# Optimization experiments

Hardware: AMD Instinct MI355X
Metric: run time of the kernel (lower is better)

The kernel has to match this reference:

```python
import jax, jax.numpy as jnp
import numpy as np

N = 10000      # nodes
E = 320000     # edges
H = 128        # hidden_features
GF = 12        # graph-level features
L = 6          # gnn layers
EPS = 1e-5


def _glorot(key, shape):
    fan_in = shape[0]
    return (jax.random.normal(key, shape, jnp.float32) / np.sqrt(fan_in)).astype(jnp.float32)


def periodic_difference(x_i, x_j, domain):
    diff = x_i - x_j
    # (1 - 2*(x_i < x_j)) * domain  ==  +domain if x_i >= x_j else -domain
    shift = jnp.where(x_i < x_j, -domain, domain)
    diff_shifted = diff - shift
    return jnp.where(jnp.abs(diff) < jnp.abs(diff_shifted), diff, diff_shifted)


def _mlp2_relu(x, W1, b1, W2, b2):
    # Linear -> ReLU -> Linear -> ReLU
    return jax.nn.relu(jax.nn.relu(x @ W1 + b1) @ W2 + b2)


def setup_inputs() -> dict:
    key = jax.random.key(0)
    ks = jax.random.split(key, 32)
    inp = {
        "v": jax.random.normal(ks[0], (N, 6), jnp.float32),
        "pos": jax.random.uniform(ks[1], (N, 3), jnp.float32),
        "r": jax.random.uniform(ks[2], (N, 1), jnp.float32),
        "domain": jnp.ones((3,), jnp.float32),
        "t": jax.random.uniform(ks[3], (1,), jnp.float32),
        "x_global": jax.random.normal(ks[4], (4,), jnp.float32),
        "domain_next": jnp.ones((3,), jnp.float32),
        "t_next": jax.random.uniform(ks[5], (1,), jnp.float32),
        "edge_index": jax.random.randint(ks[6], (2, E), 0, N, jnp.int32),
        "batch": jnp.zeros((N,), jnp.int32),
    }
    # embedding MLP: 19 -> H -> H
    inp["emb_W1"] = _glorot(ks[7], (19, H)); inp["emb_b1"] = jnp.zeros((H,), jnp.float32)
    inp["emb_W2"] = _glorot(ks[8], (H, H)); inp["emb_b2"] = jnp.zeros((H,), jnp.float32)
    # per-layer message net: 157 -> H -> H ; update net: 268 -> H -> H
    msg_in = H + GF + 3 + 2 * (6 + 1)   # 157
    upd_in = H + H + GF                 # 268
    inp["msg_W1"] = jnp.stack([_glorot(jax.random.fold_in(ks[9], i), (msg_in, H)) for i in range(L)])
    inp["msg_b1"] = jnp.zeros((L, H), jnp.float32)
    inp["msg_W2"] = jnp.stack([_glorot(jax.random.fold_in(ks[10], i), (H, H)) for i in range(L)])
    inp["msg_b2"] = jnp.zeros((L, H), jnp.float32)
    inp["upd_W1"] = jnp.stack([_glorot(jax.random.fold_in(ks[11], i), (upd_in, H)) for i in range(L)])
    inp["upd_b1"] = jnp.zeros((L, H), jnp.float32)
    inp["upd_W2"] = jnp.stack([_glorot(jax.random.fold_in(ks[12], i), (H, H)) for i in range(L)])
    inp["upd_b2"] = jnp.zeros((L, H), jnp.float32)
    # output MLP: H -> H -> 9 ; macro MLP: H -> H -> 3
    inp["out_W1"] = _glorot(ks[13], (H, H)); inp["out_b1"] = jnp.zeros((H,), jnp.float32)
    inp["out_W2"] = _glorot(ks[14], (H, 9)); inp["out_b2"] = jnp.zeros((9,), jnp.float32)
    inp["mac_W1"] = _glorot(ks[15], (H, H)); inp["mac_b1"] = jnp.zeros((H,), jnp.float32)
    inp["mac_W2"] = _glorot(ks[16], (H, 3)); inp["mac_b2"] = jnp.zeros((3,), jnp.float32)
    return inp


def reference(v, pos, r, domain, t, x_global, domain_next, t_next, edge_index, batch,
              emb_W1, emb_b1, emb_W2, emb_b2,
              msg_W1, msg_b1, msg_W2, msg_b2,
              upd_W1, upd_b1, upd_W2, upd_b2,
              out_W1, out_b1, out_W2, out_b2,
              mac_W1, mac_b1, mac_W2, mac_b2):
    n = v.shape[0]
    gf = jnp.concatenate([domain, t, x_global, domain_next, t_next])          # [12]
    gf_n = jnp.broadcast_to(gf, (n, GF))
    node_features = jnp.concatenate([pos, v], axis=1)                         # [N, 9]

    # embedding (positions excluded)
    h = _mlp2_relu(jnp.concatenate([r, v, gf_n], axis=1), emb_W1, emb_b1, emb_W2, emb_b2)

    src, dst = edge_index[0], edge_index[1]   # j = source, i = target (PyG default)
    gf_e = jnp.broadcast_to(gf, (src.shape[0], GF))
    counts = jax.ops.segment_sum(jnp.ones(src.shape, h.dtype), dst, num_segments=N)
    inv_counts = (1.0 / jnp.maximum(counts, 1.0))[:, None]

    pos_diff = periodic_difference(pos[dst], pos[src], domain)                # [E, 3]
    v_i, v_j, r_i, r_j = v[dst], v[src], r[dst], r[src]

    for l in range(L):
        h_i, h_j = h[dst], h[src]
        msg_in = jnp.concatenate([h_i - h_j, v_i, v_j, r_i, r_j, pos_diff, gf_e], axis=1)
        m = _mlp2_relu(msg_in, msg_W1[l], msg_b1[l], msg_W2[l], msg_b2[l])    # [E, H]
        agg = jax.ops.segment_sum(m, dst, num_segments=N) * inv_counts        # scatter-mean
        upd_in = jnp.concatenate([h, agg, gf_n], axis=1)
        u = _mlp2_relu(upd_in, upd_W1[l], upd_b1[l], upd_W2[l], upd_b2[l])
        h = u + h                                                              # residual (in==out)
        # InstanceNorm over each graph (single graph here), biased variance
        mu = h.mean(axis=0, keepdims=True)
        var = h.var(axis=0, keepdims=True)
        h = (h - mu) / jnp.sqrt(var + EPS)

    prediction = jax.nn.relu(h @ out_W1 + out_b1) @ out_W2 + out_b2 + node_features
    pred_x = jnp.remainder(prediction[:, :3], domain_next)
    pred_v = prediction[:, 3:]
    h_mean = h.mean(axis=0)                                                    # global mean pool, 1 graph
    pred_macro = jax.nn.relu(h_mean @ mac_W1 + mac_b1) @ mac_W2 + mac_b2
    return pred_x, pred_v, pred_macro
```

## Files before the change

kernel.cpp:

```cpp
#include <hip/hip_runtime.h>
#include <hip/hip_bf16.h>

#define NN 10000
#define NE 320000
#define HD 128
#define NL 6
#define EPSV 1e-5f

typedef _Float16 half8  __attribute__((ext_vector_type(8)));
typedef _Float16 half4v __attribute__((ext_vector_type(4)));
typedef float    f32x4  __attribute__((ext_vector_type(4)));

__device__ __forceinline__ float relu_(float x){ return fmaxf(x, 0.0f); }


__global__ void k_degree(const int* __restrict__ dst, int* __restrict__ counts){
  int e = blockIdx.x*256 + threadIdx.x;
  if (e < NE) atomicAdd(&counts[dst[e]], 1);
}

__global__ void k_scan(const int* __restrict__ counts, int* __restrict__ offs, float* __restrict__ invc){
  __shared__ int lds[1024];
  __shared__ int base_s;
  int tid = threadIdx.x;
  if (tid==0) base_s = 0;
  __syncthreads();
  for (int start=0; start<NN; start+=1024){
    int i = start+tid;
    int vv = (i<NN)? counts[i] : 0;
    lds[tid]=vv; __syncthreads();
    for (int off=1; off<1024; off<<=1){
      int t = (tid>=off)? lds[tid-off] : 0;
      __syncthreads();
      lds[tid] += t;
      __syncthreads();
    }
    int incl = lds[tid];
    if (i<NN){
      offs[i] = base_s + incl - vv;
      invc[i] = 1.0f / fmaxf((float)vv, 1.0f);
    }
    __syncthreads();
    if (tid==1023) base_s += lds[1023];
    __syncthreads();
  }
  if (tid==0) offs[NN] = base_s;
}

__global__ void k_place(const int* __restrict__ src, const int* __restrict__ dst,
                        const int* __restrict__ offs, int* __restrict__ cursor, int* __restrict__ csr){
  int e = blockIdx.x*256 + threadIdx.x;
  if (e < NE){
    int d = dst[e];
    int p = atomicAdd(&cursor[d], 1);
    csr[offs[d]+p] = src[e];
  }
}


__global__ void k_biasfold(const float* __restrict__ dom, const float* __restrict__ tt,
                           const float* __restrict__ xg, const float* __restrict__ domn,
                           const float* __restrict__ tn,
                           const float* __restrict__ embW1, const float* __restrict__ embB1,
                           const float* __restrict__ msgW1, const float* __restrict__ msgB1,
                           const float* __restrict__ updW1, const float* __restrict__ updB1,
                           float* __restrict__ b1eff, float* __restrict__ mu, float* __restrict__ rstd){
  float gf[12];
  gf[0]=dom[0]; gf[1]=dom[1]; gf[2]=dom[2]; gf[3]=tt[0];
  gf[4]=xg[0]; gf[5]=xg[1]; gf[6]=xg[2]; gf[7]=xg[3];
  gf[8]=domn[0]; gf[9]=domn[1]; gf[10]=domn[2]; gf[11]=tn[0];
  int b = blockIdx.x, t = threadIdx.x;
  if (b==0){
    float s = embB1[t];
    #pragma unroll
    for (int k=0;k<12;++k) s += gf[k]*embW1[(7+k)*HD + t];
    b1eff[t] = s;
  } else if (b<=6){
    int l=b-1;
    float s = msgB1[l*HD+t];
    #pragma unroll
    for (int k=0;k<12;++k) s += gf[k]*msgW1[((size_t)l*157 + 145+k)*HD + t];
    b1eff[(1+l)*HD + t] = s;
  } else if (b<=12){
    int l=b-7;
    float s = updB1[l*HD+t];
    #pragma unroll
    for (int k=0;k<12;++k) s += gf[k]*updW1[((size_t)l*268 + 256+k)*HD + t];
    b1eff[(7+l)*HD + t] = s;
  } else {
    mu[t] = 0.f;
    rstd[t] = 1.f;
  }
}


__global__ void k_embed(const float* __restrict__ r, const float* __restrict__ v,
                        const float* __restrict__ W1, const float* __restrict__ b1e,
                        const float* __restrict__ W2, const float* __restrict__ b2,
                        float* __restrict__ hb){
  __shared__ alignas(16) float a1s[4][HD];
  int tid=threadIdx.x, wid=tid>>6, lane=tid&63;
  int gw = blockIdx.x*4 + wid;
  int f0=lane, f1=lane+64;
  float* a1 = a1s[wid];
  float b1f0=b1e[f0], b1f1=b1e[f1], b2f0=b2[f0], b2f1=b2[f1];
  for (int n=gw*4; n<gw*4+4; ++n){
    float in7[7];
    in7[0]=r[n];
    #pragma unroll
    for (int k=0;k<6;++k) in7[1+k]=v[n*6+k];
    float z0=b1f0, z1=b1f1;
    #pragma unroll
    for (int k=0;k<7;++k){ z0 += in7[k]*W1[k*HD+f0]; z1 += in7[k]*W1[k*HD+f1]; }
    a1[f0]=relu_(z0); a1[f1]=relu_(z1);
    float h0=b2f0, h1=b2f1;
    for (int k=0;k<HD;++k){ float a=a1[k]; h0+=a*W2[k*HD+f0]; h1+=a*W2[k*HD+f1]; }
    hb[n*HD+f0]=relu_(h0); hb[n*HD+f1]=relu_(h1);
  }
}


__global__ void k_hW(const float* __restrict__ hb, const float* __restrict__ mu, const float* __restrict__ rstd,
                     const float* __restrict__ v, const float* __restrict__ r,
                     const float* __restrict__ W, const float* __restrict__ b1e,
                     float* __restrict__ P, float* __restrict__ Q){
  __shared__ alignas(16) float hs[4][HD*4];
  int tid=threadIdx.x, wid=tid>>6, lane=tid&63;
  int gw=blockIdx.x*4+wid;
  int f0=lane, f1=lane+64;
  float* h4 = hs[wid];
  int n0 = gw*4;
  float mu0=mu[f0], mu1=mu[f1], rs0=rstd[f0], rs1=rstd[f1];
  float4 hv0, hv1;
  hv0.x=(hb[(n0+0)*HD+f0]-mu0)*rs0; hv0.y=(hb[(n0+1)*HD+f0]-mu0)*rs0;
  hv0.z=(hb[(n0+2)*HD+f0]-mu0)*rs0; hv0.w=(hb[(n0+3)*HD+f0]-mu0)*rs0;
  hv1.x=(hb[(n0+0)*HD+f1]-mu1)*rs1; hv1.y=(hb[(n0+1)*HD+f1]-mu1)*rs1;
  hv1.z=(hb[(n0+2)*HD+f1]-mu1)*rs1; hv1.w=(hb[(n0+3)*HD+f1]-mu1)*rs1;
  *(float4*)&h4[f0*4]=hv0; *(float4*)&h4[f1*4]=hv1;
  float m0[4]={0,0,0,0}, m1[4]={0,0,0,0};
  for (int k=0;k<HD;++k){
    float4 a = *(const float4*)&h4[k*4];
    float w0=W[k*HD+f0], w1=W[k*HD+f1];
    m0[0]+=a.x*w0; m1[0]+=a.x*w1;
    m0[1]+=a.y*w0; m1[1]+=a.y*w1;
    m0[2]+=a.z*w0; m1[2]+=a.z*w1;
    m0[3]+=a.w*w0; m1[3]+=a.w*w1;
  }
  float wvi0[6], wvi1[6], wvj0[6], wvj1[6];
  #pragma unroll
  for (int x=0;x<6;++x){
    wvi0[x]=W[(128+x)*HD+f0]; wvi1[x]=W[(128+x)*HD+f1];
    wvj0[x]=W[(134+x)*HD+f0]; wvj1[x]=W[(134+x)*HD+f1];
  }
  float wri0=W[140*HD+f0], wri1=W[140*HD+f1];
  float wrj0=W[141*HD+f0], wrj1=W[141*HD+f1];
  float b10=b1e[f0], b11=b1e[f1];
  #pragma unroll
  for (int e=0;e<4;++e){
    int n = n0+e;
    float p0 = m0[e] + b10, p1 = m1[e] + b11;
    float q0 = -m0[e],      q1 = -m1[e];
    #pragma unroll
    for (int x=0;x<6;++x){
      float vx = v[n*6+x];
      p0 += vx*wvi0[x]; p1 += vx*wvi1[x];
      q0 += vx*wvj0[x]; q1 += vx*wvj1[x];
    }
    float rn = r[n];
    p0 += rn*wri0; p1 += rn*wri1;
    q0 += rn*wrj0; q1 += rn*wrj1;
    P[n*HD+f0]=p0; P[n*HD+f1]=p1;
    Q[n*HD+f0]=q0; Q[n*HD+f1]=q1;
  }
}


__global__ __launch_bounds__(256,2) void k_edge(
    const float* __restrict__ P, const float* __restrict__ Q,
    const float* __restrict__ pos, const float* __restrict__ dom,
    const int* __restrict__ offs, const int* __restrict__ csr,
    const float* __restrict__ Wpd, const float* __restrict__ W2, const float* __restrict__ b2,
    const float* __restrict__ invc, float* __restrict__ agg,
    float* __restrict__ zsum, float* __restrict__ zsumsq){
  __shared__ alignas(16) _Float16 w1pd[128*32];
  __shared__ alignas(16) _Float16 a1hi[16*136];
  __shared__ alignas(16) _Float16 a1lo[16*136];
  int tid = threadIdx.x;
  if (blockIdx.x==0 && tid<HD){ zsum[tid]=0.f; zsumsq[tid]=0.f; }
  if (tid < 128){
    int f = tid;
    #pragma unroll
    for (int k=0;k<32;++k) w1pd[f*32+k] = (_Float16)0.f;
    #pragma unroll
    for (int x=0;x<3;++x){
      float w = Wpd[x*HD + f];
      _Float16 h = (_Float16)w;
      w1pd[f*32 + x]     = h;
      w1pd[f*32 + 3 + x] = h;
      w1pd[f*32 + 6 + x] = (_Float16)(w - (float)h);
    }
  }
  int wid = tid>>6, lane = tid&63, g = lane>>4, c = lane&15;
  int t0 = 2*wid, t1 = 2*wid+1;
  half8 w2h[4][2], w2l[4][2];
  #pragma unroll
  for (int ks=0; ks<4; ++ks){
    #pragma unroll
    for (int tt=0; tt<2; ++tt){
      int col = 16*(2*wid+tt) + c;
      half8 fh, fl;
      #pragma unroll
      for (int j=0;j<8;++j){
        float w = W2[(ks*32 + g*8 + j)*HD + col];
        _Float16 h = (_Float16)w;
        fh[j] = h;
        fl[j] = (_Float16)(w - (float)h);
      }
      w2h[ks][tt] = fh;
      w2l[ks][tt] = fl;
    }
  }
  float b2v0 = b2[16*t0 + c], b2v1 = b2[16*t1 + c];
  float dm0=dom[0], dm1=dom[1], dm2=dom[2];
  f32x4 zero4 = {0.f,0.f,0.f,0.f};
  __syncthreads();
  int n0 = blockIdx.x*4;
  for (int n = n0; n < n0+4; ++n){
    f32x4 pv0 = *(const f32x4*)(P + (size_t)n*HD + 16*t0 + 4*g);
    f32x4 pv1 = *(const f32x4*)(P + (size_t)n*HD + 16*t1 + 4*g);
    float pn0=pos[n*3+0], pn1=pos[n*3+1], pn2=pos[n*3+2];
    float acc0=0.f, acc1=0.f;
    int ib=offs[n], ie=offs[n+1];
    for (int base=ib; base<ie; base+=16){
      int nb = ie - base; if (nb>16) nb = 16;
      int sA = csr[base + ((c<nb)? c : nb-1)];
      float q0=pos[sA*3+0], q1=pos[sA*3+1], q2=pos[sA*3+2];
      float pd0,pd1,pd2;
      { float diff,sh,ds;
        diff=pn0-q0; sh=(pn0<q0)?-dm0:dm0; ds=diff-sh; pd0=(fabsf(diff)<fabsf(ds))?diff:ds;
        diff=pn1-q1; sh=(pn1<q1)?-dm1:dm1; ds=diff-sh; pd1=(fabsf(diff)<fabsf(ds))?diff:ds;
        diff=pn2-q2; sh=(pn2<q2)?-dm2:dm2; ds=diff-sh; pd2=(fabsf(diff)<fabsf(ds))?diff:ds;
      }
      _Float16 p0h = (_Float16)pd0, p1h = (_Float16)pd1, p2h = (_Float16)pd2;
      _Float16 p0l = (_Float16)(pd0 - (float)p0h);
      _Float16 p1l = (_Float16)(pd1 - (float)p1h);
      _Float16 p2l = (_Float16)(pd2 - (float)p2h);
      half8 pdf;
      #pragma unroll
      for (int j=0;j<8;++j) pdf[j]=(_Float16)0.f;
      if (g==0){ pdf[0]=p0h; pdf[1]=p1h; pdf[2]=p2h; pdf[3]=p0l; pdf[4]=p1l; pdf[5]=p2l; pdf[6]=p0h; pdf[7]=p1h; }
      else if (g==1){ pdf[0]=p2h; }
      half8 w1f0 = *(const half8*)&w1pd[(16*t0 + c)*32 + g*8];
      half8 w1f1 = *(const half8*)&w1pd[(16*t1 + c)*32 + g*8];
      f32x4 d0 = __builtin_amdgcn_mfma_f32_16x16x32_f16(w1f0, pdf, zero4, 0,0,0);
      f32x4 d1 = __builtin_amdgcn_mfma_f32_16x16x32_f16(w1f1, pdf, zero4, 0,0,0);
      const float* Qs = Q + (size_t)sA*HD;
      f32x4 qv0 = *(const f32x4*)(Qs + 16*t0 + 4*g);
      f32x4 qv1 = *(const f32x4*)(Qs + 16*t1 + 4*g);
      half4v h0, l0, h1, l1;
      #pragma unroll
      for (int j=0;j<4;++j){
        float a = fmaxf(d0[j] + pv0[j] + qv0[j], 0.f);
        _Float16 hh = (_Float16)a;
        h0[j] = hh; l0[j] = (_Float16)(a - (float)hh);
        float b = fmaxf(d1[j] + pv1[j] + qv1[j], 0.f);
        _Float16 hb2 = (_Float16)b;
        h1[j] = hb2; l1[j] = (_Float16)(b - (float)hb2);
      }
      *(half4v*)&a1hi[c*136 + 16*t0 + 4*g] = h0;
      *(half4v*)&a1lo[c*136 + 16*t0 + 4*g] = l0;
      *(half4v*)&a1hi[c*136 + 16*t1 + 4*g] = h1;
      *(half4v*)&a1lo[c*136 + 16*t1 + 4*g] = l1;
      __syncthreads();
      f32x4 m0 = zero4, m1 = zero4;
      #pragma unroll
      for (int ks=0; ks<4; ++ks){
        half8 ah = *(const half8*)&a1hi[c*136 + ks*32 + g*8];
        half8 al = *(const half8*)&a1lo[c*136 + ks*32 + g*8];
        m0 = __builtin_amdgcn_mfma_f32_16x16x32_f16(ah, w2h[ks][0], m0, 0,0,0);
        m0 = __builtin_amdgcn_mfma_f32_16x16x32_f16(al, w2h[ks][0], m0, 0,0,0);
        m0 = __builtin_amdgcn_mfma_f32_16x16x32_f16(ah, w2l[ks][0], m0, 0,0,0);
        m1 = __builtin_amdgcn_mfma_f32_16x16x32_f16(ah, w2h[ks][1], m1, 0,0,0);
        m1 = __builtin_amdgcn_mfma_f32_16x16x32_f16(al, w2h[ks][1], m1, 0,0,0);
        m1 = __builtin_amdgcn_mfma_f32_16x16x32_f16(ah, w2l[ks][1], m1, 0,0,0);
      }
      if (nb == 16){
        acc0 += fmaxf(m0[0]+b2v0,0.f)+fmaxf(m0[1]+b2v0,0.f)+fmaxf(m0[2]+b2v0,0.f)+fmaxf(m0[3]+b2v0,0.f);
        acc1 += fmaxf(m1[0]+b2v1,0.f)+fmaxf(m1[1]+b2v1,0.f)+fmaxf(m1[2]+b2v1,0.f)+fmaxf(m1[3]+b2v1,0.f);
      } else {
        #pragma unroll
        for (int j=0;j<4;++j){
          if (4*g+j < nb){
            acc0 += fmaxf(m0[j]+b2v0, 0.f);
            acc1 += fmaxf(m1[j]+b2v1, 0.f);
          }
        }
      }
      __syncthreads();
    }
    acc0 += __shfl_xor(acc0, 16); acc0 += __shfl_xor(acc0, 32);
    acc1 += __shfl_xor(acc1, 16); acc1 += __shfl_xor(acc1, 32);
    if (g==0){
      float ic = invc[n];
      agg[n*HD + 16*t0 + c] = acc0*ic;
      agg[n*HD + 16*t1 + c] = acc1*ic;
    }
  }
}


__global__ __launch_bounds__(512,1) void k_upd(
    float* __restrict__ hb, const float* __restrict__ mu, const float* __restrict__ rstd,
    const float* __restrict__ agg,
    const float* __restrict__ U1, const float* __restrict__ b1e,
    const float* __restrict__ U2, const float* __restrict__ bs2,
    float* __restrict__ sum, float* __restrict__ sumsq){
  __shared__ alignas(16) _Float16 Xhi[16*264];
  __shared__ alignas(16) _Float16 Xlo[16*264];
  __shared__ alignas(16) _Float16 Ahi[16*136];
  __shared__ alignas(16) _Float16 Alo[16*136];
  int tid = threadIdx.x;
  int n0 = blockIdx.x*16;
  {
    int node = tid>>5, chunk = tid&31;
    int n = n0 + node;
    int f = chunk*8;
    half8 xh, xl;
    if (f < 128){
      #pragma unroll
      for (int j=0;j<8;++j){
        float x = (hb[(size_t)n*HD + f+j] - mu[f+j]) * rstd[f+j];
        _Float16 h = (_Float16)x;
        xh[j] = h; xl[j] = (_Float16)(x - (float)h);
      }
    } else {
      #pragma unroll
      for (int j=0;j<8;++j){
        float x = agg[(size_t)n*HD + (f-128)+j];
        _Float16 h = (_Float16)x;
        xh[j] = h; xl[j] = (_Float16)(x - (float)h);
      }
    }
    *(half8*)&Xhi[node*264 + f] = xh;
    *(half8*)&Xlo[node*264 + f] = xl;
  }
  int wid = tid>>6, lane = tid&63, g = lane>>4, c = lane&15;
  int col = 16*wid + c;
  half8 b1h[8], b1l[8], b2h[4], b2l[4];
  #pragma unroll
  for (int ks=0; ks<8; ++ks){
    half8 fh, fl;
    #pragma unroll
    for (int j=0;j<8;++j){
      float w = U1[(size_t)(ks*32 + g*8 + j)*HD + col];
      _Float16 h = (_Float16)w;
      fh[j]=h; fl[j]=(_Float16)(w - (float)h);
    }
    b1h[ks]=fh; b1l[ks]=fl;
  }
  #pragma unroll
  for (int ks=0; ks<4; ++ks){
    half8 fh, fl;
    #pragma unroll
    for (int j=0;j<8;++j){
      float w = U2[(size_t)(ks*32 + g*8 + j)*HD + col];
      _Float16 h = (_Float16)w;
      fh[j]=h; fl[j]=(_Float16)(w - (float)h);
    }
    b2h[ks]=fh; b2l[ks]=fl;
  }
  f32x4 zero4 = {0.f,0.f,0.f,0.f};
  __syncthreads();
  f32x4 d = zero4;
  #pragma unroll
  for (int ks=0; ks<8; ++ks){
    half8 ah = *(const half8*)&Xhi[c*264 + ks*32 + g*8];
    half8 al = *(const half8*)&Xlo[c*264 + ks*32 + g*8];
    d = __builtin_amdgcn_mfma_f32_16x16x32_f16(ah, b1h[ks], d, 0,0,0);
    d = __builtin_amdgcn_mfma_f32_16x16x32_f16(al, b1h[ks], d, 0,0,0);
    d = __builtin_amdgcn_mfma_f32_16x16x32_f16(ah, b1l[ks], d, 0,0,0);
  }
  {
    float bb = b1e[col];
    #pragma unroll
    for (int jj=0;jj<4;++jj){
      float a = fmaxf(d[jj] + bb, 0.f);
      _Float16 h = (_Float16)a;
      Ahi[(g*4+jj)*136 + col] = h;
      Alo[(g*4+jj)*136 + col] = (_Float16)(a - (float)h);
    }
  }
  __syncthreads();
  f32x4 u = zero4;
  #pragma unroll
  for (int ks=0; ks<4; ++ks){
    half8 ah = *(const half8*)&Ahi[c*136 + ks*32 + g*8];
    half8 al = *(const half8*)&Alo[c*136 + ks*32 + g*8];
    u = __builtin_amdgcn_mfma_f32_16x16x32_f16(ah, b2h[ks], u, 0,0,0);
    u = __builtin_amdgcn_mfma_f32_16x16x32_f16(al, b2h[ks], u, 0,0,0);
    u = __builtin_amdgcn_mfma_f32_16x16x32_f16(ah, b2l[ks], u, 0,0,0);
  }
  float bc = bs2[col];
  float mc = mu[col], rc = rstd[col];
  float s=0.f, q=0.f;
  #pragma unroll
  for (int jj=0;jj<4;++jj){
    int n = n0 + g*4 + jj;
    float hn = (hb[(size_t)n*HD + col] - mc)*rc;
    float b0 = hn + fmaxf(u[jj] + bc, 0.f);
    hb[(size_t)n*HD + col] = b0;
    s += b0; q += b0*b0;
  }
  s += __shfl_xor(s,16); s += __shfl_xor(s,32);
  q += __shfl_xor(q,16); q += __shfl_xor(q,32);
  if (g==0){
    atomicAdd(&sum[col], s);
    atomicAdd(&sumsq[col], q);
  }
}

__global__ void k_normfin(const float* __restrict__ sum, const float* __restrict__ sumsq,
                          float* __restrict__ mu, float* __restrict__ rstd){
  int t=threadIdx.x;
  float m = sum[t]*(1.0f/NN);
  float var = sumsq[t]*(1.0f/NN) - m*m;
  mu[t]=m;
  rstd[t]=rsqrtf(fmaxf(var,0.0f)+EPSV);
}


__global__ void k_out(const float* __restrict__ hb, const float* __restrict__ mu, const float* __restrict__ rstd,
                      const float* __restrict__ pos, const float* __restrict__ v,
                      const float* __restrict__ W1, const float* __restrict__ b1,
                      const float* __restrict__ W2, const float* __restrict__ b2,
                      const float* __restrict__ domn, float* __restrict__ out){
  __shared__ alignas(16) float hs[4][HD*4];
  __shared__ alignas(16) float a1s[4][HD*4];
  int tid=threadIdx.x, wid=tid>>6, lane=tid&63;
  int gw=blockIdx.x*4+wid;
  int f0=lane, f1=lane+64;
  float* h4=hs[wid];
  float* a1p=a1s[wid];
  int n0=gw*4;
  float mu0=mu[f0], mu1=mu[f1], rs0=rstd[f0], rs1=rstd[f1];
  float4 hv0,hv1;
  hv0.x=(hb[(n0+0)*HD+f0]-mu0)*rs0; hv0.y=(hb[(n0+1)*HD+f0]-mu0)*rs0;
  hv0.z=(hb[(n0+2)*HD+f0]-mu0)*rs0; hv0.w=(hb[(n0+3)*HD+f0]-mu0)*rs0;
  hv1.x=(hb[(n0+0)*HD+f1]-mu1)*rs1; hv1.y=(hb[(n0+1)*HD+f1]-mu1)*rs1;
  hv1.z=(hb[(n0+2)*HD+f1]-mu1)*rs1; hv1.w=(hb[(n0+3)*HD+f1]-mu1)*rs1;
  *(float4*)&h4[f0*4]=hv0; *(float4*)&h4[f1*4]=hv1;
  float b1f0=b1[f0], b1f1=b1[f1];
  float zf0[4]={b1f0,b1f0,b1f0,b1f0}, zf1[4]={b1f1,b1f1,b1f1,b1f1};
  for (int k=0;k<HD;++k){
    float4 a = *(const float4*)&h4[k*4];
    float w0=W1[k*HD+f0], w1=W1[k*HD+f1];
    zf0[0]+=a.x*w0; zf1[0]+=a.x*w1;
    zf0[1]+=a.y*w0; zf1[1]+=a.y*w1;
    zf0[2]+=a.z*w0; zf1[2]+=a.z*w1;
    zf0[3]+=a.w*w0; zf1[3]+=a.w*w1;
  }
  *(float4*)&a1p[f0*4] = make_float4(relu_(zf0[0]),relu_(zf0[1]),relu_(zf0[2]),relu_(zf0[3]));
  *(float4*)&a1p[f1*4] = make_float4(relu_(zf1[0]),relu_(zf1[1]),relu_(zf1[2]),relu_(zf1[3]));
  if (lane < 36){
    int e = lane/9, j = lane - e*9;
    int n = n0+e;
    float p = b2[j];
    for (int k=0;k<HD;++k) p += a1p[k*4+e]*W2[k*9+j];
    if (j<3){
      p += pos[n*3+j];
      float d = domn[j];
      p = p - floorf(p/d)*d;
      out[n*3+j] = p;
    } else {
      p += v[n*6 + (j-3)];
      out[3*NN + n*6 + (j-3)] = p;
    }
  }
}

__global__ void k_macro(const float* __restrict__ sum, const float* __restrict__ mu, const float* __restrict__ rstd,
                        const float* __restrict__ W1, const float* __restrict__ b1,
                        const float* __restrict__ W2, const float* __restrict__ b2,
                        float* __restrict__ out){
  __shared__ float hm[HD];
  __shared__ float as[HD];
  int t=threadIdx.x;
  hm[t] = (sum[t]*(1.0f/NN) - mu[t])*rstd[t];
  __syncthreads();
  float z=b1[t];
  for (int k=0;k<HD;++k) z += hm[k]*W1[k*HD+t];
  as[t]=relu_(z);
  __syncthreads();
  if (t<3){
    float p=b2[t];
    for (int k=0;k<HD;++k) p += as[k]*W2[k*3+t];
    out[9*NN+t]=p;
  }
}


extern "C" void kernel_launch(void* const* d_in, const int* in_sizes, int n_in,
                              void* d_out, int out_size, void* d_ws, size_t ws_size,
                              hipStream_t stream) {
  const float* v    = (const float*)d_in[0];
  const float* pos  = (const float*)d_in[1];
  const float* r    = (const float*)d_in[2];
  const float* dom  = (const float*)d_in[3];
  const float* tt   = (const float*)d_in[4];
  const float* xg   = (const float*)d_in[5];
  const float* domn = (const float*)d_in[6];
  const float* tn   = (const float*)d_in[7];
  const int*   eidx = (const int*)d_in[8];
  const float* embW1 = (const float*)d_in[10];
  const float* embB1 = (const float*)d_in[11];
  const float* embW2 = (const float*)d_in[12];
  const float* embB2 = (const float*)d_in[13];
  const float* msgW1 = (const float*)d_in[14];
  const float* msgB1 = (const float*)d_in[15];
  const float* msgW2 = (const float*)d_in[16];
  const float* msgB2 = (const float*)d_in[17];
  const float* updW1 = (const float*)d_in[18];
  const float* updB1 = (const float*)d_in[19];
  const float* updW2 = (const float*)d_in[20];
  const float* updB2 = (const float*)d_in[21];
  const float* outW1 = (const float*)d_in[22];
  const float* outB1 = (const float*)d_in[23];
  const float* outW2 = (const float*)d_in[24];
  const float* outB2 = (const float*)d_in[25];
  const float* macW1 = (const float*)d_in[26];
  const float* macB1 = (const float*)d_in[27];
  const float* macW2 = (const float*)d_in[28];
  const float* macB2 = (const float*)d_in[29];
  float* out = (float*)d_out;
  float* ws  = (float*)d_ws;

  float* hb    = ws;
  float* P     = ws + 1280000;
  float* Q     = ws + 2560000;
  float* agg   = ws + 3840000;
  float* invc  = ws + 5120000;
  float* b1eff = ws + 5130000;
  float* sum   = ws + 5131664;
  float* sumsq = ws + 5131792;
  float* mu    = ws + 5131920;
  float* rstd  = ws + 5132048;
  int* counts  = (int*)(ws + 5132304);
  int* offs    = counts + NN;
  int* cursor  = offs + NN + 1;
  int* csr     = cursor + NN;

  const int* srcA = eidx;
  const int* dstA = eidx + NE;

  hipMemsetAsync(counts, 0, NN*sizeof(int), stream);
  hipMemsetAsync(cursor, 0, NN*sizeof(int), stream);

  k_degree<<<(NE+255)/256, 256, 0, stream>>>(dstA, counts);
  k_scan<<<1, 1024, 0, stream>>>(counts, offs, invc);
  k_place<<<(NE+255)/256, 256, 0, stream>>>(srcA, dstA, offs, cursor, csr);
  k_biasfold<<<14, 128, 0, stream>>>(dom, tt, xg, domn, tn, embW1, embB1, msgW1, msgB1, updW1, updB1,
                                     b1eff, mu, rstd);
  k_embed<<<625, 256, 0, stream>>>(r, v, embW1, b1eff, embW2, embB2, hb);

  for (int l=0; l<NL; ++l){
    k_hW<<<625,256,0,stream>>>(hb, mu, rstd, v, r, msgW1 + (size_t)l*157*HD, b1eff + (1+l)*HD, P, Q);
    k_edge<<<2500,256,0,stream>>>(P, Q, pos, dom, offs, csr,
        msgW1 + ((size_t)l*157+142)*HD,
        msgW2 + (size_t)l*HD*HD, msgB2 + l*HD, invc, agg, sum, sumsq);
    k_upd<<<625,512,0,stream>>>(hb, mu, rstd, agg,
        updW1 + (size_t)l*268*HD, b1eff + (7+l)*HD,
        updW2 + (size_t)l*HD*HD, updB2 + l*HD, sum, sumsq);
    k_normfin<<<1,128,0,stream>>>(sum, sumsq, mu, rstd);
  }

  k_out<<<625,256,0,stream>>>(hb, mu, rstd, pos, v, outW1, outB1, outW2, outB2, domn, out);
  k_macro<<<1,128,0,stream>>>(sum, mu, rstd, macW1, macB1, macW2, macB2, out);
}
```

Measured before the change: 876.3 us.

## Port node h@W1 projection to split-fp16 MFMA and pad edge weight LDS

Rewrites k_hW so each 512-thread block handles 16 nodes. The normalized hidden state is staged in LDS as hi/lo fp16 pairs, and the 128x128 projection runs on 16x16x32 MFMA with three products to keep near-fp32 accuracy. This replaces the scalar FMA loop over 4 nodes per wave. Separately, it pads the w1pd LDS row stride in k_edge from 32 to 40 halves to reduce bank conflicts on the half8 fragment loads. The split-precision scheme adds MFMA work and conversion overhead, and the one-tile-per-block layout may limit reuse of the weight fragments.

Result: faster. 855.6 us (-2.4%).

```diff
diff --git a/kernel.cpp b/kernel.cpp
--- a/kernel.cpp
+++ b/kernel.cpp
@@ -120,57 +120,76 @@
 }
 
 
-__global__ void k_hW(const float* __restrict__ hb, const float* __restrict__ mu, const float* __restrict__ rstd,
-                     const float* __restrict__ v, const float* __restrict__ r,
-                     const float* __restrict__ W, const float* __restrict__ b1e,
-                     float* __restrict__ P, float* __restrict__ Q){
-  __shared__ alignas(16) float hs[4][HD*4];
-  int tid=threadIdx.x, wid=tid>>6, lane=tid&63;
-  int gw=blockIdx.x*4+wid;
-  int f0=lane, f1=lane+64;
-  float* h4 = hs[wid];
-  int n0 = gw*4;
-  float mu0=mu[f0], mu1=mu[f1], rs0=rstd[f0], rs1=rstd[f1];
-  float4 hv0, hv1;
-  hv0.x=(hb[(n0+0)*HD+f0]-mu0)*rs0; hv0.y=(hb[(n0+1)*HD+f0]-mu0)*rs0;
-  hv0.z=(hb[(n0+2)*HD+f0]-mu0)*rs0; hv0.w=(hb[(n0+3)*HD+f0]-mu0)*rs0;
-  hv1.x=(hb[(n0+0)*HD+f1]-mu1)*rs1; hv1.y=(hb[(n0+1)*HD+f1]-mu1)*rs1;
-  hv1.z=(hb[(n0+2)*HD+f1]-mu1)*rs1; hv1.w=(hb[(n0+3)*HD+f1]-mu1)*rs1;
-  *(float4*)&h4[f0*4]=hv0; *(float4*)&h4[f1*4]=hv1;
-  float m0[4]={0,0,0,0}, m1[4]={0,0,0,0};
-  for (int k=0;k<HD;++k){
-    float4 a = *(const float4*)&h4[k*4];
-    float w0=W[k*HD+f0], w1=W[k*HD+f1];
-    m0[0]+=a.x*w0; m1[0]+=a.x*w1;
-    m0[1]+=a.y*w0; m1[1]+=a.y*w1;
-    m0[2]+=a.z*w0; m1[2]+=a.z*w1;
-    m0[3]+=a.w*w0; m1[3]+=a.w*w1;
-  }
-  float wvi0[6], wvi1[6], wvj0[6], wvj1[6];
+__global__ __launch_bounds__(512,1) void k_hW(
+    const float* __restrict__ hb, const float* __restrict__ mu, const float* __restrict__ rstd,
+    const float* __restrict__ v, const float* __restrict__ r,
+    const float* __restrict__ W, const float* __restrict__ b1e,
+    float* __restrict__ P, float* __restrict__ Q){
+  __shared__ alignas(16) _Float16 Xhi[16*136];
+  __shared__ alignas(16) _Float16 Xlo[16*136];
+  int tid = threadIdx.x;
+  int n0 = blockIdx.x*16;
+  if (tid < 256){
+    int node = tid>>4, chunk = tid&15;
+    int n = n0 + node;
+    int f = chunk*8;
+    half8 xh, xl;
+    #pragma unroll
+    for (int j=0;j<8;++j){
+      float x = (hb[(size_t)n*HD + f+j] - mu[f+j]) * rstd[f+j];
+      _Float16 h = (_Float16)x;
+      xh[j] = h; xl[j] = (_Float16)(x - (float)h);
+    }
+    *(half8*)&Xhi[node*136 + f] = xh;
+    *(half8*)&Xlo[node*136 + f] = xl;
+  }
+  int wid = tid>>6, lane = tid&63, g = lane>>4, c = lane&15;
+  int col = 16*wid + c;
+  half8 bh[4], bl[4];
+  #pragma unroll
+  for (int ks=0; ks<4; ++ks){
+    half8 fh, fl;
+    #pragma unroll
+    for (int j=0;j<8;++j){
+      float w = W[(size_t)(ks*32 + g*8 + j)*HD + col];
+      _Float16 h = (_Float16)w;
+      fh[j]=h; fl[j]=(_Float16)(w - (float)h);
+    }
+    bh[ks]=fh; bl[ks]=fl;
+  }
+  float wvi[6], wvj[6];
   #pragma unroll
   for (int x=0;x<6;++x){
-    wvi0[x]=W[(128+x)*HD+f0]; wvi1[x]=W[(128+x)*HD+f1];
-    wvj0[x]=W[(134+x)*HD+f0]; wvj1[x]=W[(134+x)*HD+f1];
-  }
-  float wri0=W[140*HD+f0], wri1=W[140*HD+f1];
-  float wrj0=W[141*HD+f0], wrj1=W[141*HD+f1];
-  float b10=b1e[f0], b11=b1e[f1];
-  #pragma unroll
-  for (int e=0;e<4;++e){
-    int n = n0+e;
-    float p0 = m0[e] + b10, p1 = m1[e] + b11;
-    float q0 = -m0[e],      q1 = -m1[e];
+    wvi[x]=W[(size_t)(128+x)*HD+col];
+    wvj[x]=W[(size_t)(134+x)*HD+col];
+  }
+  float wri=W[(size_t)140*HD+col], wrj=W[(size_t)141*HD+col];
+  float b1c=b1e[col];
+  f32x4 zero4 = {0.f,0.f,0.f,0.f};
+  __syncthreads();
+  f32x4 d = zero4;
+  #pragma unroll
+  for (int ks=0; ks<4; ++ks){
+    half8 ah = *(const half8*)&Xhi[c*136 + ks*32 + g*8];
+    half8 al = *(const half8*)&Xlo[c*136 + ks*32 + g*8];
+    d = __builtin_amdgcn_mfma_f32_16x16x32_f16(ah, bh[ks], d, 0,0,0);
+    d = __builtin_amdgcn_mfma_f32_16x16x32_f16(al, bh[ks], d, 0,0,0);
+    d = __builtin_amdgcn_mfma_f32_16x16x32_f16(ah, bl[ks], d, 0,0,0);
+  }
+  #pragma unroll
+  for (int jj=0;jj<4;++jj){
+    int n = n0 + g*4 + jj;
+    float m = d[jj];
+    float p = m + b1c, q = -m;
     #pragma unroll
     for (int x=0;x<6;++x){
       float vx = v[n*6+x];
-      p0 += vx*wvi0[x]; p1 += vx*wvi1[x];
-      q0 += vx*wvj0[x]; q1 += vx*wvj1[x];
+      p += vx*wvi[x]; q += vx*wvj[x];
     }
     float rn = r[n];
-    p0 += rn*wri0; p1 += rn*wri1;
-    q0 += rn*wrj0; q1 += rn*wrj1;
-    P[n*HD+f0]=p0; P[n*HD+f1]=p1;
-    Q[n*HD+f0]=q0; Q[n*HD+f1]=q1;
+    p += rn*wri; q += rn*wrj;
+    P[(size_t)n*HD+col]=p;
+    Q[(size_t)n*HD+col]=q;
   }
 }
 
@@ -182,7 +201,7 @@
     const float* __restrict__ Wpd, const float* __restrict__ W2, const float* __restrict__ b2,
     const float* __restrict__ invc, float* __restrict__ agg,
     float* __restrict__ zsum, float* __restrict__ zsumsq){
-  __shared__ alignas(16) _Float16 w1pd[128*32];
+  __shared__ alignas(16) _Float16 w1pd[128*40];
   __shared__ alignas(16) _Float16 a1hi[16*136];
   __shared__ alignas(16) _Float16 a1lo[16*136];
   int tid = threadIdx.x;
@@ -190,14 +209,14 @@
   if (tid < 128){
     int f = tid;
     #pragma unroll
-    for (int k=0;k<32;++k) w1pd[f*32+k] = (_Float16)0.f;
+    for (int k=0;k<32;++k) w1pd[f*40+k] = (_Float16)0.f;
     #pragma unroll
     for (int x=0;x<3;++x){
       float w = Wpd[x*HD + f];
       _Float16 h = (_Float16)w;
-      w1pd[f*32 + x]     = h;
-      w1pd[f*32 + 3 + x] = h;
-      w1pd[f*32 + 6 + x] = (_Float16)(w - (float)h);
+      w1pd[f*40 + x]     = h;
+      w1pd[f*40 + 3 + x] = h;
+      w1pd[f*40 + 6 + x] = (_Float16)(w - (float)h);
     }
   }
   int wid = tid>>6, lane = tid&63, g = lane>>4, c = lane&15;
@@ -250,8 +269,8 @@
       for (int j=0;j<8;++j) pdf[j]=(_Float16)0.f;
       if (g==0){ pdf[0]=p0h; pdf[1]=p1h; pdf[2]=p2h; pdf[3]=p0l; pdf[4]=p1l; pdf[5]=p2l; pdf[6]=p0h; pdf[7]=p1h; }
       else if (g==1){ pdf[0]=p2h; }
-      half8 w1f0 = *(const half8*)&w1pd[(16*t0 + c)*32 + g*8];
-      half8 w1f1 = *(const half8*)&w1pd[(16*t1 + c)*32 + g*8];
+      half8 w1f0 = *(const half8*)&w1pd[(16*t0 + c)*40 + g*8];
+      half8 w1f1 = *(const half8*)&w1pd[(16*t1 + c)*40 + g*8];
       f32x4 d0 = __builtin_amdgcn_mfma_f32_16x16x32_f16(w1f0, pdf, zero4, 0,0,0);
       f32x4 d1 = __builtin_amdgcn_mfma_f32_16x16x32_f16(w1f1, pdf, zero4, 0,0,0);
       const float* Qs = Q + (size_t)sA*HD;
@@ -563,7 +582,7 @@
   k_embed<<<625, 256, 0, stream>>>(r, v, embW1, b1eff, embW2, embB2, hb);
 
   for (int l=0; l<NL; ++l){
-    k_hW<<<625,256,0,stream>>>(hb, mu, rstd, v, r, msgW1 + (size_t)l*157*HD, b1eff + (1+l)*HD, P, Q);
+    k_hW<<<625,512,0,stream>>>(hb, mu, rstd, v, r, msgW1 + (size_t)l*157*HD, b1eff + (1+l)*HD, P, Q);
     k_edge<<<2500,256,0,stream>>>(P, Q, pos, dom, offs, csr,
         msgW1 + ((size_t)l*157+142)*HD,
         msgW2 + (size_t)l*HD*HD, msgB2 + l*HD, invc, agg, sum, sumsq);
```
